# Kernel tuning notes

Hardware: AMD Instinct MI355X
Metric: run time of the kernel (lower is better)

Reference implementation:

```python
import jax, jax.numpy as jnp
import numpy as np

B, N = 256, 128000

def setup_inputs() -> dict:
    key = jax.random.key(0)
    k1, k2, k3 = jax.random.split(key, 3)
    logits = jax.random.normal(k1, (B, N), dtype=jnp.float32) * 4.0
    k = jax.random.randint(k2, (B,), 1, 1000, dtype=jnp.int32)
    p = jax.random.uniform(k3, (B,), dtype=jnp.float32, minval=0.05, maxval=0.99)
    return {"logits": logits, "k": k, "p": p}


def reference(logits, k, p):
    """Faithful jax version of original_apply_top_k_top_p (k and p both given).
    Sort ascending, mask everything below the k-th largest, then mask the
    low-probability prefix whose cumulative softmax mass is <= 1-p, and
    scatter the masked sorted logits back to original positions."""
    Bn, Nn = logits.shape
    k = jnp.clip(k, 1, Nn)
    idx = jnp.argsort(logits, axis=-1)                       # ascending order
    logits_sort = jnp.take_along_axis(logits, idx, axis=-1)
    neg_inf = jnp.float32(-jnp.inf)

    # --- top-k: threshold = value at position (N - k) in ascending order ---
    kth_pos = (Nn - k).astype(jnp.int32)[:, None]            # [B,1]
    kth_val = jnp.take_along_axis(logits_sort, kth_pos, axis=-1)
    logits_sort = jnp.where(logits_sort < kth_val, neg_inf, logits_sort)

    # --- top-p on the (top-k masked) sorted logits ---
    probs = jax.nn.softmax(logits_sort, axis=-1)
    probs_sum = jnp.cumsum(probs, axis=-1)
    top_p_mask = probs_sum <= (1.0 - p)[:, None]
    top_p_mask = top_p_mask.at[:, -1].set(False)             # always keep argmax
    logits_sort = jnp.where(top_p_mask, neg_inf, logits_sort)

    # --- scatter back to original vocabulary positions ---
    rows = jnp.arange(Bn)[:, None]
    out = jnp.empty_like(logits).at[rows, idx].set(logits_sort)
    return out
```

## Files before the change

kernel.cpp:

```cpp
#include <hip/hip_runtime.h>
#include <stdint.h>
#include <math.h>

#define BB 256
#define NN 128000
#define N4 (NN / 4)
#define CAP 2048
#define BLK 1024
#define THRESH 9.0f
#define LBUF_CAP 512
#define MASK_BITS 0xFF7F0000u
#define BF16_FINITE_LIM 3.0e38f

#define CTR_STRIDE 4
#define WS_NEEDED ((size_t)4096 + (size_t)BB * CAP * sizeof(uint2))

typedef float f4v __attribute__((ext_vector_type(4)));

__device__ __forceinline__ uint32_t fkey_enc(uint32_t bits) {
  return (bits & 0x80000000u) ? ~bits : (bits | 0x80000000u);
}
__device__ __forceinline__ float fkey_dec(uint32_t fkey) {
  uint32_t bits = (fkey & 0x80000000u) ? (fkey ^ 0x80000000u) : ~fkey;
  return __uint_as_float(bits);
}

__global__ void k0_zero(uint32_t* counters) {
  int t = threadIdx.x;
  if (t < BB * CTR_STRIDE) counters[t] = 0u;
}

__global__ __launch_bounds__(256) void kGather(
    const float* __restrict__ logits, uint32_t* __restrict__ counters,
    uint2* __restrict__ pairs) {
  const int row = blockIdx.y;
  __shared__ uint2 lbuf[LBUF_CAP];
  __shared__ uint32_t lcount;
  __shared__ uint32_t gbase;
  if (threadIdx.x == 0) lcount = 0u;
  __syncthreads();

  const f4v* in4 = (const f4v*)(logits + (size_t)row * NN);
  const int g = blockIdx.x * 256 + (int)threadIdx.x;
  const bool tail_ok = (g + 3 * 8192) < N4;

  f4v v[4];
#pragma unroll
  for (int j = 0; j < 3; ++j) v[j] = in4[g + j * 8192];
  if (tail_ok) v[3] = in4[g + 3 * 8192];
  __builtin_amdgcn_sched_barrier(0);

#pragma unroll
  for (int j = 0; j < 4; ++j) {
    if (j == 3 && !tail_ok) break;
    const int col0 = (g + j * 8192) * 4;
#pragma unroll
    for (int e = 0; e < 4; ++e) {
      float x = v[j][e];
      if (x > THRESH) {
        uint32_t slot = atomicAdd(&lcount, 1u);
        if (slot < LBUF_CAP)
          lbuf[slot] = make_uint2(fkey_enc(__float_as_uint(x)),
                                  (uint32_t)(col0 + e));
      }
    }
  }
  __syncthreads();

  uint32_t n = lcount;
  if (threadIdx.x == 0) {
    if (n > LBUF_CAP) {
      atomicAdd(&counters[(size_t)row * CTR_STRIDE], (uint32_t)(CAP + 1));
      gbase = 0xFFFFFFFFu;
    } else {
      gbase = atomicAdd(&counters[(size_t)row * CTR_STRIDE], n);
    }
  }
  __syncthreads();
  uint32_t base = gbase;
  if (base == 0xFFFFFFFFu) return;
  for (uint32_t i = threadIdx.x; i < n; i += 256) {
    uint32_t s = base + i;
    if (s < CAP) pairs[(size_t)row * CAP + s] = lbuf[i];
  }
}

__global__ __launch_bounds__(BLK) void kB_finalize(
    const float* __restrict__ logits, const int* __restrict__ kin,
    const float* __restrict__ pin, const uint32_t* __restrict__ counters,
    const uint2* __restrict__ pairs, float* __restrict__ out) {
  const int row = blockIdx.x;
  const int tid = threadIdx.x;

  __shared__ unsigned long long skey[CAP];
  __shared__ double dbuf[2][BLK];
  __shared__ uint32_t red[BLK];
  __shared__ uint32_t scount;

  {
    const float MASKV = __uint_as_float(MASK_BITS);
    const f4v mask4 = {MASKV, MASKV, MASKV, MASKV};
    f4v* out4 = (f4v*)(out + (size_t)row * NN);
    for (int i = tid; i < N4; i += BLK) out4[i] = mask4;
  }

  int k = kin[row];
  if (k < 1) k = 1;
  if (k > NN) k = NN;
  uint32_t c = counters[(size_t)row * CTR_STRIDE];

  if (c <= CAP && c >= (uint32_t)k) {
    for (int i = tid; i < (int)c; i += BLK) {
      uint2 pr = pairs[(size_t)row * CAP + i];
      skey[i] = ((unsigned long long)pr.x << 32) | (unsigned long long)pr.y;
    }
  } else {
    const float* rowp = logits + (size_t)row * NN;
    uint32_t lo = 0u, hi = 0xFFFFFFFFu;
    while (lo < hi) {
      uint32_t mid = (uint32_t)(((uint64_t)lo + (uint64_t)hi + 1ull) >> 1);
      uint32_t cnt = 0;
      for (int i = tid; i < NN; i += BLK)
        cnt += (fkey_enc(__float_as_uint(rowp[i])) >= mid) ? 1u : 0u;
      red[tid] = cnt;
      __syncthreads();
      for (int off = BLK / 2; off > 0; off >>= 1) {
        if (tid < off) red[tid] += red[tid + off];
        __syncthreads();
      }
      uint32_t total = red[0];
      __syncthreads();
      if (total >= (uint32_t)k) lo = mid;
      else hi = mid - 1u;
    }
    if (tid == 0) scount = 0u;
    __syncthreads();
    for (int i = tid; i < NN; i += BLK) {
      uint32_t fk = fkey_enc(__float_as_uint(rowp[i]));
      if (fk >= lo) {
        uint32_t slot = atomicAdd(&scount, 1u);
        if (slot < CAP) skey[slot] = ((unsigned long long)fk << 32) | (uint32_t)i;
      }
    }
    __syncthreads();
    c = scount;
    if (c > CAP) c = CAP;
  }
  if (c == 0u) return;
  if ((uint32_t)k > c) k = (int)c;

  for (int i = (int)c + tid; i < CAP; i += BLK) skey[i] = 0ull;
  __syncthreads();
  for (int kk = 2; kk <= CAP; kk <<= 1) {
    for (int j = kk >> 1; j > 0; j >>= 1) {
      for (int i = tid; i < CAP; i += BLK) {
        int ixj = i ^ j;
        if (ixj > i) {
          unsigned long long a = skey[i], b = skey[ixj];
          bool up = ((i & kk) == 0);
          if (up ? (a > b) : (a < b)) {
            skey[i] = b;
            skey[ixj] = a;
          }
        }
      }
      __syncthreads();
    }
  }

  const uint32_t mfkey = (uint32_t)(skey[CAP - 1] >> 32);
  const uint32_t kthfkey = (uint32_t)(skey[CAP - k] >> 32);
  const double mval = (double)fkey_dec(mfkey);
  const int base = CAP - (int)c;
  const float p = pin[row];
  const double lim_frac = (double)(1.0f - p);

  double loc[2];
  double chunk = 0.0;
#pragma unroll
  for (int j = 0; j < 2; ++j) {
    int i = tid * 2 + j;
    double e = 0.0;
    if (i >= base) {
      uint32_t fk = (uint32_t)(skey[i] >> 32);
      if (fk >= kthfkey) e = exp((double)fkey_dec(fk) - mval);
    }
    chunk += e;
    loc[j] = chunk;
  }
  dbuf[0][tid] = chunk;
  __syncthreads();
  int src = 0;
  for (int off = 1; off < BLK; off <<= 1) {
    double v = dbuf[src][tid];
    if (tid >= off) v += dbuf[src][tid - off];
    dbuf[src ^ 1][tid] = v;
    src ^= 1;
    __syncthreads();
  }
  const double S = dbuf[src][BLK - 1];
  const double lim = lim_frac * S;
  const double excl = (tid == 0) ? 0.0 : dbuf[src][tid - 1];

#pragma unroll
  for (int j = 0; j < 2; ++j) {
    int i = tid * 2 + j;
    if (i >= base) {
      unsigned long long sk = skey[i];
      uint32_t fk = (uint32_t)(sk >> 32);
      if (fk >= kthfkey) {
        double A = excl + loc[j];
        if (A > lim) {
          uint32_t col = (uint32_t)(sk & 0xFFFFFFFFull);
          float v = fkey_dec(fk);
          if (col < NN && isfinite(v) && fabsf(v) < BF16_FINITE_LIM)
            out[(size_t)row * NN + col] = v;
        }
      }
    }
  }
}

__global__ __launch_bounds__(BLK) void topk_topp_row(
    const float* __restrict__ logits, const int* __restrict__ kin,
    const float* __restrict__ pin, float* __restrict__ out) {
  const int row = blockIdx.x;
  const int tid = threadIdx.x;
  __shared__ unsigned long long skey[CAP];
  __shared__ double dbuf[2][BLK];
  __shared__ uint32_t red[BLK];
  __shared__ uint32_t scount;
  if (tid == 0) scount = 0u;
  __syncthreads();
  const float MASKV = __uint_as_float(MASK_BITS);
  const float4 mask4 = make_float4(MASKV, MASKV, MASKV, MASKV);
  const float4* in4 = (const float4*)(logits + (size_t)row * NN);
  float4* out4 = (float4*)(out + (size_t)row * NN);
  for (int c4 = tid; c4 < N4; c4 += BLK) {
    float4 v = in4[c4];
    out4[c4] = mask4;
    float vals[4] = {v.x, v.y, v.z, v.w};
#pragma unroll
    for (int j = 0; j < 4; ++j) {
      if (vals[j] > THRESH) {
        uint32_t slot = atomicAdd(&scount, 1u);
        if (slot < CAP)
          skey[slot] = ((unsigned long long)fkey_enc(__float_as_uint(vals[j])) << 32) |
                       (unsigned long long)(uint32_t)(c4 * 4 + j);
      }
    }
  }
  __syncthreads();
  int k = kin[row];
  if (k < 1) k = 1;
  if (k > NN) k = NN;
  uint32_t c = scount;
  if (c > CAP || c < (uint32_t)k) {
    const float* rowp = logits + (size_t)row * NN;
    uint32_t lo = 0u, hi = 0xFFFFFFFFu;
    while (lo < hi) {
      uint32_t mid = (uint32_t)(((uint64_t)lo + (uint64_t)hi + 1ull) >> 1);
      uint32_t cnt = 0;
      for (int i = tid; i < NN; i += BLK)
        cnt += (fkey_enc(__float_as_uint(rowp[i])) >= mid) ? 1u : 0u;
      red[tid] = cnt;
      __syncthreads();
      for (int off = BLK / 2; off > 0; off >>= 1) {
        if (tid < off) red[tid] += red[tid + off];
        __syncthreads();
      }
      uint32_t total = red[0];
      __syncthreads();
      if (total >= (uint32_t)k) lo = mid;
      else hi = mid - 1u;
    }
    if (tid == 0) scount = 0u;
    __syncthreads();
    for (int i = tid; i < NN; i += BLK) {
      uint32_t fk = fkey_enc(__float_as_uint(rowp[i]));
      if (fk >= lo) {
        uint32_t slot = atomicAdd(&scount, 1u);
        if (slot < CAP) skey[slot] = ((unsigned long long)fk << 32) | (uint32_t)i;
      }
    }
    __syncthreads();
    c = scount;
    if (c > CAP) c = CAP;
  }
  if (c == 0u) return;
  if ((uint32_t)k > c) k = (int)c;
  for (int i = (int)c + tid; i < CAP; i += BLK) skey[i] = 0ull;
  __syncthreads();
  for (int kk = 2; kk <= CAP; kk <<= 1) {
    for (int j = kk >> 1; j > 0; j >>= 1) {
      for (int i = tid; i < CAP; i += BLK) {
        int ixj = i ^ j;
        if (ixj > i) {
          unsigned long long a = skey[i], b = skey[ixj];
          bool up = ((i & kk) == 0);
          if (up ? (a > b) : (a < b)) {
            skey[i] = b;
            skey[ixj] = a;
          }
        }
      }
      __syncthreads();
    }
  }
  const uint32_t mfkey = (uint32_t)(skey[CAP - 1] >> 32);
  const uint32_t kthfkey = (uint32_t)(skey[CAP - k] >> 32);
  const double mval = (double)fkey_dec(mfkey);
  const int base = CAP - (int)c;
  const float p = pin[row];
  const double lim_frac = (double)(1.0f - p);
  double loc[2];
  double chunk = 0.0;
#pragma unroll
  for (int j = 0; j < 2; ++j) {
    int i = tid * 2 + j;
    double e = 0.0;
    if (i >= base) {
      uint32_t fk = (uint32_t)(skey[i] >> 32);
      if (fk >= kthfkey) e = exp((double)fkey_dec(fk) - mval);
    }
    chunk += e;
    loc[j] = chunk;
  }
  dbuf[0][tid] = chunk;
  __syncthreads();
  int src = 0;
  for (int off = 1; off < BLK; off <<= 1) {
    double v = dbuf[src][tid];
    if (tid >= off) v += dbuf[src][tid - off];
    dbuf[src ^ 1][tid] = v;
    src ^= 1;
    __syncthreads();
  }
  const double S = dbuf[src][BLK - 1];
  const double lim = lim_frac * S;
  const double excl = (tid == 0) ? 0.0 : dbuf[src][tid - 1];
#pragma unroll
  for (int j = 0; j < 2; ++j) {
    int i = tid * 2 + j;
    if (i >= base) {
      unsigned long long sk = skey[i];
      uint32_t fk = (uint32_t)(sk >> 32);
      if (fk >= kthfkey) {
        double A = excl + loc[j];
        if (A > lim) {
          uint32_t col = (uint32_t)(sk & 0xFFFFFFFFull);
          float v = fkey_dec(fk);
          if (col < NN && isfinite(v) && fabsf(v) < BF16_FINITE_LIM)
            out[(size_t)row * NN + col] = v;
        }
      }
    }
  }
}

extern "C" void kernel_launch(void* const* d_in, const int* in_sizes, int n_in,
                              void* d_out, int out_size, void* d_ws, size_t ws_size,
                              hipStream_t stream) {
  const float* logits = (const float*)d_in[0];
  const int* kk = (const int*)d_in[1];
  const float* pp = (const float*)d_in[2];
  float* out = (float*)d_out;
  (void)in_sizes; (void)n_in; (void)out_size;

  if (ws_size >= WS_NEEDED) {
    uint32_t* counters = (uint32_t*)d_ws;
    uint2* pairs = (uint2*)((char*)d_ws + 4096);
    k0_zero<<<1, 1024, 0, stream>>>(counters);
    dim3 gG(32, BB);
    kGather<<<gG, 256, 0, stream>>>(logits, counters, pairs);
    kB_finalize<<<BB, BLK, 0, stream>>>(logits, kk, pp, counters, pairs, out);
  } else {
    topk_topp_row<<<BB, BLK, 0, stream>>>(logits, kk, pp, out);
  }
}
```

Baseline: 84.91 us.

## Move output fill and counter zeroing to memsets, retile gather into contiguous chunks

Replaces the counter-zeroing kernel with hipMemsetAsync, and moves the per-row mask fill of the output from the finalize kernel into a device-wide hipMemsetD32Async. The gather kernel now uses 25 contiguous chunks per row, each with 5 exact float4 loads per thread, instead of 32 strided blocks with a tail check. The aim is to take the serial per-row output fill off the 256-block finalize kernel and to make the gather loads contiguous with no tail branch. It adds a separate full-output memset pass that stays in the timed stream.

```diff
diff --git a/kernel.cpp b/kernel.cpp
--- a/kernel.cpp
+++ b/kernel.cpp
@@ -9,6 +9,8 @@
 #define BLK 1024
 #define THRESH 9.0f
 #define LBUF_CAP 512
+#define CHUNKS_PER_ROW 25
+#define CHUNK_F4 (N4 / CHUNKS_PER_ROW)
 #define MASK_BITS 0xFF7F0000u
 #define BF16_FINITE_LIM 3.0e38f
 
@@ -23,11 +25,6 @@
 __device__ __forceinline__ float fkey_dec(uint32_t fkey) {
   uint32_t bits = (fkey & 0x80000000u) ? (fkey ^ 0x80000000u) : ~fkey;
   return __uint_as_float(bits);
-}
-
-__global__ void k0_zero(uint32_t* counters) {
-  int t = threadIdx.x;
-  if (t < BB * CTR_STRIDE) counters[t] = 0u;
 }
 
 __global__ __launch_bounds__(256) void kGather(
@@ -40,31 +37,40 @@
   if (threadIdx.x == 0) lcount = 0u;
   __syncthreads();
 
+  const int t = (int)threadIdx.x;
+  const int base = (int)blockIdx.x * CHUNK_F4;
   const f4v* in4 = (const f4v*)(logits + (size_t)row * NN);
-  const int g = blockIdx.x * 256 + (int)threadIdx.x;
-  const bool tail_ok = (g + 3 * 8192) < N4;
-
-  f4v v[4];
-#pragma unroll
-  for (int j = 0; j < 3; ++j) v[j] = in4[g + j * 8192];
-  if (tail_ok) v[3] = in4[g + 3 * 8192];
+
+  const f4v v0 = in4[base + t];
+  const f4v v1 = in4[base + t + 256];
+  const f4v v2 = in4[base + t + 512];
+  const f4v v3 = in4[base + t + 768];
+  const f4v v4 = in4[base + t + 1024];
   __builtin_amdgcn_sched_barrier(0);
 
-#pragma unroll
-  for (int j = 0; j < 4; ++j) {
-    if (j == 3 && !tail_ok) break;
-    const int col0 = (g + j * 8192) * 4;
-#pragma unroll
-    for (int e = 0; e < 4; ++e) {
-      float x = v[j][e];
-      if (x > THRESH) {
-        uint32_t slot = atomicAdd(&lcount, 1u);
-        if (slot < LBUF_CAP)
-          lbuf[slot] = make_uint2(fkey_enc(__float_as_uint(x)),
-                                  (uint32_t)(col0 + e));
-      }
-    }
-  }
+#define PUSHC(x, colexpr)                                            \
+  do {                                                               \
+    if ((x) > THRESH) {                                              \
+      uint32_t slot = atomicAdd(&lcount, 1u);                        \
+      if (slot < LBUF_CAP)                                           \
+        lbuf[slot] = make_uint2(fkey_enc(__float_as_uint(x)),        \
+                                (uint32_t)(colexpr));                \
+    }                                                                \
+  } while (0)
+#define CONSUME4(vv, fbase)                                          \
+  do {                                                               \
+    PUSHC((vv).x, (fbase) * 4 + 0);                                  \
+    PUSHC((vv).y, (fbase) * 4 + 1);                                  \
+    PUSHC((vv).z, (fbase) * 4 + 2);                                  \
+    PUSHC((vv).w, (fbase) * 4 + 3);                                  \
+  } while (0)
+  CONSUME4(v0, base + t);
+  CONSUME4(v1, base + t + 256);
+  CONSUME4(v2, base + t + 512);
+  CONSUME4(v3, base + t + 768);
+  CONSUME4(v4, base + t + 1024);
+#undef CONSUME4
+#undef PUSHC
   __syncthreads();
 
   uint32_t n = lcount;
@@ -77,10 +83,10 @@
     }
   }
   __syncthreads();
-  uint32_t base = gbase;
-  if (base == 0xFFFFFFFFu) return;
+  uint32_t gb = gbase;
+  if (gb == 0xFFFFFFFFu) return;
   for (uint32_t i = threadIdx.x; i < n; i += 256) {
-    uint32_t s = base + i;
+    uint32_t s = gb + i;
     if (s < CAP) pairs[(size_t)row * CAP + s] = lbuf[i];
   }
 }
@@ -96,13 +102,6 @@
   __shared__ double dbuf[2][BLK];
   __shared__ uint32_t red[BLK];
   __shared__ uint32_t scount;
-
-  {
-    const float MASKV = __uint_as_float(MASK_BITS);
-    const f4v mask4 = {MASKV, MASKV, MASKV, MASKV};
-    f4v* out4 = (f4v*)(out + (size_t)row * NN);
-    for (int i = tid; i < N4; i += BLK) out4[i] = mask4;
-  }
 
   int k = kin[row];
   if (k < 1) k = 1;
@@ -370,8 +369,10 @@
   if (ws_size >= WS_NEEDED) {
     uint32_t* counters = (uint32_t*)d_ws;
     uint2* pairs = (uint2*)((char*)d_ws + 4096);
-    k0_zero<<<1, 1024, 0, stream>>>(counters);
-    dim3 gG(32, BB);
+    hipMemsetAsync(d_ws, 0, 4096, stream);
+    hipMemsetD32Async((hipDeviceptr_t)out, (int)MASK_BITS,
+                      (size_t)BB * NN, stream);
+    dim3 gG(CHUNKS_PER_ROW, BB);
     kGather<<<gG, 256, 0, stream>>>(logits, counters, pairs);
     kB_finalize<<<BB, BLK, 0, stream>>>(logits, kk, pp, counters, pairs, out);
   } else {
```

Result: slower. 87.02 us (+2.5%).
